# Optimization experiments

Measured on AMD Instinct MI355X. Metric: run time of the kernel, lower is better.

## Reference

```python
import jax, jax.numpy as jnp
import numpy as np

B, S, E, H, DH, W = 2, 4096, 1024, 16, 64, 512
NB = S // W          # number of query blocks
U = 2 * W            # key block = previous block + current block
INIT = 0.02


def setup_inputs() -> dict:
    key = jax.random.key(0)
    ks = jax.random.split(key, 6)
    x = jax.random.normal(ks[0], (B, S, E), jnp.float32)
    bias = jax.random.normal(ks[1], (H, W), jnp.float32)  # per-head alibi over rel. distance 0..W-1
    Wq = INIT * jax.random.normal(ks[2], (E, H, DH), jnp.float32)
    Wk = INIT * jax.random.normal(ks[3], (E, DH), jnp.float32)   # MQA: single shared K head
    Wv = INIT * jax.random.normal(ks[4], (E, DH), jnp.float32)   # MQA: single shared V head
    Wo = INIT * jax.random.normal(ks[5], (H, DH, E), jnp.float32)
    return {"x": x, "bias": bias, "Wq": Wq, "Wk": Wk, "Wv": Wv, "Wo": Wo}


def _sliding_window_attn(q, k, v, bias):
    # q: [B,S,H,DH]; k,v: [B,S,DH] (shared across heads); bias: [H,W]
    scale = 1.0 / np.sqrt(DH)
    qb = q.reshape(B, NB, W, H, DH)
    # pad one window of zeros in front so every query block sees a 'previous' block
    kp = jnp.pad(k, ((0, 0), (W, 0), (0, 0)))
    vp = jnp.pad(v, ((0, 0), (W, 0), (0, 0)))
    idx = jnp.arange(NB)[:, None] * W + jnp.arange(U)[None, :]  # [NB,U] into padded seq
    kb = kp[:, idx]  # [B,NB,U,DH]
    vb = vp[:, idx]  # [B,NB,U,DH]
    # scores over (query-in-block w, key-in-2W-block u)
    scores = jnp.einsum('bnwhd,bnud->bhnwu', qb, kb) * scale  # [B,H,NB,W,U]
    t = jnp.arange(W)
    u = jnp.arange(U)
    d = t[:, None] - u[None, :] + W                 # relative distance i-j, [W,U]
    rel_ok = (d >= 0) & (d < W)                     # causal + within window
    j_global = idx - W                              # global key position, [NB,U]
    valid = rel_ok[None, :, :] & (j_global >= 0)[:, None, :]  # [NB,W,U]
    bmat = bias[:, jnp.clip(d, 0, W - 1)]           # [H,W,U]
    scores = scores + bmat[None, :, None, :, :]
    neg = jnp.finfo(scores.dtype).min / 2
    scores = jnp.where(valid[None, None], scores, neg)
    p = jax.nn.softmax(scores, axis=-1)
    out = jnp.einsum('bhnwu,bnud->bnwhd', p, vb)    # [B,NB,W,H,DH]
    return out.reshape(B, S, H, DH)


def reference(x, bias, Wq, Wk, Wv, Wo):
    q = jnp.einsum('bse,ehd->bshd', x, Wq)
    k = jnp.einsum('bse,ed->bsd', x, Wk)
    v = jnp.einsum('bse,ed->bsd', x, Wv)
    attn = _sliding_window_attn(q, k, v, bias)
    return jnp.einsum('bshd,hde->bse', attn, Wo)
```

## Files before the change

kernel.cpp:

```cpp
#include <hip/hip_runtime.h>

#define Bx 2
#define Sx 4096
#define Ex 1024
#define Hx 16
#define DHx 64
#define Wwin 512

typedef unsigned short u16;
typedef unsigned int u32;
typedef __attribute__((ext_vector_type(8))) short bf16x8;
typedef __attribute__((ext_vector_type(4))) float f32x4;
typedef __attribute__((ext_vector_type(4))) unsigned short u16x4;

__device__ __forceinline__ u16 f2b(float f) {
  unsigned u = __builtin_bit_cast(unsigned, f);
  unsigned r = (u + 0x7FFFu + ((u >> 16) & 1u)) >> 16;
  return (u16)r;
}

__device__ __forceinline__ u32 cvt_pk_bf16(float lo, float hi) {
  u32 r;
  asm("v_cvt_pk_bf16_f32 %0, %1, %2" : "=v"(r) : "v"(lo), "v"(hi));
  return r;
}

__device__ __forceinline__ void gload_lds16(const void* g, void* l) {
  __builtin_amdgcn_global_load_lds(
      (const __attribute__((address_space(1))) void*)g,
      (__attribute__((address_space(3))) void*)l, 16, 0, 0);
}

__global__ __launch_bounds__(256) void cast_x_kernel(const float* __restrict__ x,
                                                     u16* __restrict__ xb) {
  long idx = ((long)blockIdx.x * 256 + threadIdx.x) * 4;
  float4 v = *(const float4*)(x + idx);
  u16x4 o;
  o[0] = f2b(v.x); o[1] = f2b(v.y); o[2] = f2b(v.z); o[3] = f2b(v.w);
  *(u16x4*)(xb + idx) = o;
}

__global__ __launch_bounds__(256) void pack_w_kernel(const float* __restrict__ Wq,
                                                     const float* __restrict__ Wk,
                                                     const float* __restrict__ Wv,
                                                     const float* __restrict__ Wo,
                                                     u16* __restrict__ wcat,
                                                     u16* __restrict__ wot) {
  int idx = blockIdx.x * 256 + threadIdx.x;
  if (idx < 1048576) {
    int e = idx >> 10, n = idx & 1023;
    wcat[n * 1024 + e] = f2b(Wq[idx]);
  } else if (idx < 1048576 + 65536) {
    int i2 = idx - 1048576;
    int e = i2 >> 6, d = i2 & 63;
    wcat[(1024 + d) * 1024 + e] = f2b(Wk[i2]);
  } else if (idx < 1048576 + 131072) {
    int i2 = idx - (1048576 + 65536);
    int e = i2 >> 6, d = i2 & 63;
    wcat[(1088 + d) * 1024 + e] = f2b(Wv[i2]);
  } else {
    int i2 = idx - (1048576 + 131072);
    int hd = i2 >> 10, e = i2 & 1023;
    wot[e * 1024 + hd] = f2b(Wo[i2]);
  }
}

template <typename OutT>
__global__ __launch_bounds__(256) void gemm_bt_kernel(const u16* __restrict__ A,
                                                      const u16* __restrict__ Bt,
                                                      OutT* __restrict__ C,
                                                      int M, int N, int K) {
  __shared__ u16 As[128 * 64];
  __shared__ u16 Bs[128 * 64];
  const int tid = threadIdx.x;
  const int lane = tid & 63, wave = tid >> 6;
  const int ll = lane & 15, gl = lane >> 4;
  const int wr = wave >> 1, wc = wave & 1;
  const long m0 = (long)blockIdx.x * 128;
  const long n0 = (long)blockIdx.y * 128;
  const int segrow = lane >> 3, cph = lane & 7;

  f32x4 acc[4][4] = {};

  for (int kb = 0; kb < K; kb += 64) {
    __syncthreads();
#pragma unroll
    for (int q = 0; q < 4; ++q) {
      int s = wave * 4 + q;
      int row = s * 8 + segrow;
      int clog = cph ^ (row & 7);
      gload_lds16(A + (m0 + row) * K + kb + clog * 8, (char*)As + s * 1024);
      gload_lds16(Bt + (n0 + row) * K + kb + clog * 8, (char*)Bs + s * 1024);
    }
    __syncthreads();
#pragma unroll
    for (int kx = 0; kx < 2; ++kx) {
      bf16x8 af[4], bfr[4];
#pragma unroll
      for (int rg = 0; rg < 4; ++rg) {
        int row = wr * 64 + rg * 16 + ll;
        int c = kx * 4 + gl;
        af[rg] = *(const bf16x8*)&As[row * 64 + ((c ^ (row & 7)) << 3)];
      }
#pragma unroll
      for (int cg = 0; cg < 4; ++cg) {
        int row = wc * 64 + cg * 16 + ll;
        int c = kx * 4 + gl;
        bfr[cg] = *(const bf16x8*)&Bs[row * 64 + ((c ^ (row & 7)) << 3)];
      }
#pragma unroll
      for (int rg = 0; rg < 4; ++rg)
#pragma unroll
        for (int cg = 0; cg < 4; ++cg)
          acc[rg][cg] = __builtin_amdgcn_mfma_f32_16x16x32_bf16(af[rg], bfr[cg],
                                                                acc[rg][cg], 0, 0, 0);
    }
  }
#pragma unroll
  for (int rg = 0; rg < 4; ++rg)
#pragma unroll
    for (int cg = 0; cg < 4; ++cg)
#pragma unroll
      for (int r = 0; r < 4; ++r) {
        long row = m0 + wr * 64 + rg * 16 + gl * 4 + r;
        long col = n0 + wc * 64 + cg * 16 + ll;
        if constexpr (sizeof(OutT) == 2)
          C[row * (long)N + col] = f2b(acc[rg][cg][r]);
        else
          C[row * (long)N + col] = acc[rg][cg][r];
      }
}

__global__ __launch_bounds__(256) void vt_transpose_kernel(const u16* __restrict__ qkvb,
                                                           u16* __restrict__ vt) {
  __shared__ u16 T[64 * 65];
  const int blk = blockIdx.x;
  const int b = blk >> 6;
  const int j0 = (blk & 63) * 64;
  const int tid = threadIdx.x;
#pragma unroll
  for (int rep = 0; rep < 16; ++rep) {
    int idx = rep * 256 + tid;
    int jj = idx >> 6, dd = idx & 63;
    T[dd * 65 + jj] = qkvb[((long)b * Sx + j0 + jj) * 1152 + 1088 + dd];
  }
  __syncthreads();
#pragma unroll
  for (int rep = 0; rep < 16; ++rep) {
    int idx = rep * 256 + tid;
    int dd = idx >> 6, jj = idx & 63;
    vt[((long)b * 64 + dd) * Sx + j0 + jj] = T[dd * 65 + jj];
  }
}

__global__ __launch_bounds__(256) void attn_kernel(const u16* __restrict__ qkv,
                                                   const u16* __restrict__ vt,
                                                   const float* __restrict__ bias,
                                                   u16* __restrict__ attnb) {
  __shared__ u16 Pb[4][32 * 64];
  __shared__ float bias2S[512];

  const int bid0 = blockIdx.x;
  const int bid = (bid0 & 7) * 128 + (bid0 >> 3);
  const int h = bid & 15;
  const int qt = (bid >> 4) & 31;
  const int b = bid >> 9;
  const int q0 = qt * 128;
  const long bS = (long)b * Sx;

  const int tid = threadIdx.x;
  const int lane = tid & 63, wave = tid >> 6;
  const int ll = lane & 15, gl = lane >> 4;
  const int wq0 = q0 + wave * 32;

  for (int i = tid; i < 512; i += 256)
    bias2S[i] = fmaf(bias[h * 512 + i], 1.4426950408889634f, -24.0f);
  __syncthreads();

  const float C1 = 0.125f * 1.4426950408889634f;

  bf16x8 qf[2][2];
#pragma unroll
  for (int rg = 0; rg < 2; ++rg)
#pragma unroll
    for (int kx = 0; kx < 2; ++kx)
      qf[rg][kx] = *(const bf16x8*)&qkv[(bS + wq0 + rg * 16 + ll) * 1152 +
                                        h * 64 + kx * 32 + gl * 8];

  u16 ov = (ll == 0) ? (u16)0x3F80 : (u16)0;
  bf16x8 vones;
#pragma unroll
  for (int i = 0; i < 8; ++i) vones[i] = (short)ov;

  f32x4 oacc[2][4] = {};
  f32x4 lacc[2] = {};

  u16* Pw = &Pb[wave][0];

  const int kb_start = (wq0 > 511) ? ((wq0 - 511) & ~63) : 0;
  const int kb_last = (wq0 + 31) & ~63;
  for (int kb = kb_start; kb <= kb_last; kb += 64) {
    bf16x8 kf[2][4], vfr[2][4];
#pragma unroll
    for (int kx = 0; kx < 2; ++kx)
#pragma unroll
      for (int cg = 0; cg < 4; ++cg) {
        kf[kx][cg] = *(const bf16x8*)&qkv[(bS + kb + cg * 16 + ll) * 1152 + 1024 +
                                          kx * 32 + gl * 8];
        vfr[kx][cg] = *(const bf16x8*)&vt[((long)b * 64 + cg * 16 + ll) * Sx + kb +
                                          kx * 32 + gl * 8];
      }
    f32x4 sacc[2][4] = {};
#pragma unroll
    for (int kx = 0; kx < 2; ++kx)
#pragma unroll
      for (int rg = 0; rg < 2; ++rg)
#pragma unroll
        for (int cg = 0; cg < 4; ++cg)
          sacc[rg][cg] = __builtin_amdgcn_mfma_f32_16x16x32_bf16(qf[rg][kx], kf[kx][cg],
                                                                 sacc[rg][cg], 0, 0, 0);
    const int dbase = (wq0 - kb) + gl * 4 - ll;
    const bool full = (kb - wq0 >= -480) && (kb - wq0 <= -64);
    if (full) {
      const float* bp = bias2S + dbase;
#pragma unroll
      for (int rg = 0; rg < 2; ++rg)
#pragma unroll
        for (int cg = 0; cg < 4; ++cg)
#pragma unroll
          for (int r = 0; r < 4; ++r)
            sacc[rg][cg][r] =
                __builtin_exp2f(fmaf(sacc[rg][cg][r], C1, bp[rg * 16 + r - cg * 16]));
    } else {
#pragma unroll
      for (int rg = 0; rg < 2; ++rg)
#pragma unroll
        for (int cg = 0; cg < 4; ++cg)
#pragma unroll
          for (int r = 0; r < 4; ++r) {
            int d = dbase + rg * 16 + r - cg * 16;
            int dc = d < 0 ? 0 : (d > 511 ? 511 : d);
            float p = __builtin_exp2f(fmaf(sacc[rg][cg][r], C1, bias2S[dc]));
            sacc[rg][cg][r] = ((unsigned)d < 512u) ? p : 0.0f;
          }
    }
#pragma unroll
    for (int rg = 0; rg < 2; ++rg)
#pragma unroll
      for (int cg = 0; cg < 4; ++cg)
#pragma unroll
        for (int rp = 0; rp < 2; ++rp) {
          u32 pk = cvt_pk_bf16(sacc[rg][cg][2 * rp], sacc[rg][cg][2 * rp + 1]);
          int row0 = rg * 16 + gl * 4 + 2 * rp;
          int col = cg * 16 + ll;
          Pw[row0 * 64 + (((col >> 3) ^ (row0 & 7)) << 3) + (col & 7)] = (u16)pk;
          int row1 = row0 + 1;
          Pw[row1 * 64 + (((col >> 3) ^ (row1 & 7)) << 3) + (col & 7)] = (u16)(pk >> 16);
        }
#pragma unroll
    for (int kx = 0; kx < 2; ++kx) {
      bf16x8 pf[2];
#pragma unroll
      for (int rg = 0; rg < 2; ++rg) {
        int row = rg * 16 + ll;
        int c = kx * 4 + gl;
        pf[rg] = *(const bf16x8*)&Pw[row * 64 + ((c ^ (row & 7)) << 3)];
      }
#pragma unroll
      for (int rg = 0; rg < 2; ++rg) {
#pragma unroll
        for (int cg = 0; cg < 4; ++cg)
          oacc[rg][cg] = __builtin_amdgcn_mfma_f32_16x16x32_bf16(pf[rg], vfr[kx][cg],
                                                                 oacc[rg][cg], 0, 0, 0);
        lacc[rg] = __builtin_amdgcn_mfma_f32_16x16x32_bf16(pf[rg], vones,
                                                           lacc[rg], 0, 0, 0);
      }
    }
  }
#pragma unroll
  for (int rg = 0; rg < 2; ++rg)
#pragma unroll
    for (int r = 0; r < 4; ++r) {
      float l = __shfl(lacc[rg][r], lane & 48);
      float inv = 1.0f / l;
      long i = wq0 + rg * 16 + gl * 4 + r;
#pragma unroll
      for (int cg = 0; cg < 4; ++cg)
        attnb[(bS + i) * 1024 + h * 64 + cg * 16 + ll] = f2b(oacc[rg][cg][r] * inv);
    }
}

extern "C" void kernel_launch(void* const* d_in, const int* in_sizes, int n_in,
                              void* d_out, int out_size, void* d_ws, size_t ws_size,
                              hipStream_t stream) {
  const float* x    = (const float*)d_in[0];
  const float* bias = (const float*)d_in[1];
  const float* Wq   = (const float*)d_in[2];
  const float* Wk   = (const float*)d_in[3];
  const float* Wv   = (const float*)d_in[4];
  const float* Wo   = (const float*)d_in[5];
  float* out = (float*)d_out;

  u16* xb    = (u16*)d_ws;
  u16* wcat  = xb    + (size_t)8192 * 1024;
  u16* wot   = wcat  + (size_t)1152 * 1024;
  u16* qkvb  = wot   + (size_t)1024 * 1024;
  u16* vtb   = qkvb  + (size_t)8192 * 1152;
  u16* attnb = xb;

  cast_x_kernel<<<8192, 256, 0, stream>>>(x, xb);
  pack_w_kernel<<<8704, 256, 0, stream>>>(Wq, Wk, Wv, Wo, wcat, wot);
  gemm_bt_kernel<u16><<<dim3(64, 9), 256, 0, stream>>>(xb, wcat, qkvb, 8192, 1152, 1024);
  vt_transpose_kernel<<<128, 256, 0, stream>>>(qkvb, vtb);
  attn_kernel<<<1024, 256, 0, stream>>>(qkvb, vtb, bias, attnb);
  gemm_bt_kernel<float><<<dim3(64, 8), 256, 0, stream>>>(attnb, wot, out, 8192, 1024, 1024);
}
```

Measured before the change: 231.0 us.

## Double-buffer GEMM LDS tiles and stage shared K/V tiles through LDS in attention

```diff
diff --git a/kernel.cpp b/kernel.cpp
--- a/kernel.cpp
+++ b/kernel.cpp
@@ -70,8 +70,8 @@
                                                       const u16* __restrict__ Bt,
                                                       OutT* __restrict__ C,
                                                       int M, int N, int K) {
-  __shared__ u16 As[128 * 64];
-  __shared__ u16 Bs[128 * 64];
+  __shared__ u16 As[2][128 * 64];
+  __shared__ u16 Bs[2][128 * 64];
   const int tid = threadIdx.x;
   const int lane = tid & 63, wave = tid >> 6;
   const int ll = lane & 15, gl = lane >> 4;
@@ -81,18 +81,26 @@
   const int segrow = lane >> 3, cph = lane & 7;
 
   f32x4 acc[4][4] = {};
-
-  for (int kb = 0; kb < K; kb += 64) {
-    __syncthreads();
-#pragma unroll
-    for (int q = 0; q < 4; ++q) {
-      int s = wave * 4 + q;
-      int row = s * 8 + segrow;
-      int clog = cph ^ (row & 7);
-      gload_lds16(A + (m0 + row) * K + kb + clog * 8, (char*)As + s * 1024);
-      gload_lds16(Bt + (n0 + row) * K + kb + clog * 8, (char*)Bs + s * 1024);
-    }
-    __syncthreads();
+  const int nt = K >> 6;
+
+#define GEMM_STAGE(buf, kb)                                                     \
+  {                                                                             \
+    _Pragma("unroll") for (int q = 0; q < 4; ++q) {                             \
+      int s = wave * 4 + q;                                                     \
+      int row = s * 8 + segrow;                                                 \
+      int clog = cph ^ (row & 7);                                               \
+      gload_lds16(A + (m0 + row) * K + (kb) + clog * 8,                         \
+                  (char*)&As[buf][0] + s * 1024);                               \
+      gload_lds16(Bt + (n0 + row) * K + (kb) + clog * 8,                        \
+                  (char*)&Bs[buf][0] + s * 1024);                               \
+    }                                                                           \
+  }
+
+  GEMM_STAGE(0, 0);
+  __syncthreads();
+  int cur = 0;
+  for (int t = 0; t < nt; ++t) {
+    if (t + 1 < nt) GEMM_STAGE(cur ^ 1, (t + 1) * 64);
 #pragma unroll
     for (int kx = 0; kx < 2; ++kx) {
       bf16x8 af[4], bfr[4];
@@ -100,13 +108,13 @@
       for (int rg = 0; rg < 4; ++rg) {
         int row = wr * 64 + rg * 16 + ll;
         int c = kx * 4 + gl;
-        af[rg] = *(const bf16x8*)&As[row * 64 + ((c ^ (row & 7)) << 3)];
+        af[rg] = *(const bf16x8*)&As[cur][row * 64 + ((c ^ (row & 7)) << 3)];
       }
 #pragma unroll
       for (int cg = 0; cg < 4; ++cg) {
         int row = wc * 64 + cg * 16 + ll;
         int c = kx * 4 + gl;
-        bfr[cg] = *(const bf16x8*)&Bs[row * 64 + ((c ^ (row & 7)) << 3)];
+        bfr[cg] = *(const bf16x8*)&Bs[cur][row * 64 + ((c ^ (row & 7)) << 3)];
       }
 #pragma unroll
       for (int rg = 0; rg < 4; ++rg)
@@ -115,7 +123,10 @@
           acc[rg][cg] = __builtin_amdgcn_mfma_f32_16x16x32_bf16(af[rg], bfr[cg],
                                                                 acc[rg][cg], 0, 0, 0);
     }
-  }
+    __syncthreads();
+    cur ^= 1;
+  }
+#undef GEMM_STAGE
 #pragma unroll
   for (int rg = 0; rg < 4; ++rg)
 #pragma unroll
@@ -157,6 +168,8 @@
                                                    const u16* __restrict__ vt,
                                                    const float* __restrict__ bias,
                                                    u16* __restrict__ attnb) {
+  __shared__ u16 Ks[2][64 * 64];
+  __shared__ u16 Vts[2][64 * 64];
   __shared__ u16 Pb[4][32 * 64];
   __shared__ float bias2S[512];
 
@@ -172,10 +185,10 @@
   const int lane = tid & 63, wave = tid >> 6;
   const int ll = lane & 15, gl = lane >> 4;
   const int wq0 = q0 + wave * 32;
+  const int segrow = lane >> 3, cph = lane & 7;
 
   for (int i = tid; i < 512; i += 256)
     bias2S[i] = fmaf(bias[h * 512 + i], 1.4426950408889634f, -24.0f);
-  __syncthreads();
 
   const float C1 = 0.125f * 1.4426950408889634f;
 
@@ -197,86 +210,114 @@
 
   u16* Pw = &Pb[wave][0];
 
-  const int kb_start = (wq0 > 511) ? ((wq0 - 511) & ~63) : 0;
-  const int kb_last = (wq0 + 31) & ~63;
-  for (int kb = kb_start; kb <= kb_last; kb += 64) {
-    bf16x8 kf[2][4], vfr[2][4];
-#pragma unroll
-    for (int kx = 0; kx < 2; ++kx)
-#pragma unroll
-      for (int cg = 0; cg < 4; ++cg) {
-        kf[kx][cg] = *(const bf16x8*)&qkv[(bS + kb + cg * 16 + ll) * 1152 + 1024 +
-                                          kx * 32 + gl * 8];
-        vfr[kx][cg] = *(const bf16x8*)&vt[((long)b * 64 + cg * 16 + ll) * Sx + kb +
-                                          kx * 32 + gl * 8];
-      }
-    f32x4 sacc[2][4] = {};
-#pragma unroll
-    for (int kx = 0; kx < 2; ++kx)
+#define ATTN_STAGE(buf, kb)                                                     \
+  {                                                                             \
+    _Pragma("unroll") for (int q = 0; q < 2; ++q) {                             \
+      int s = wave * 2 + q;                                                     \
+      int rrow = s * 8 + segrow;                    \
+      int clog = cph ^ (rrow & 7);                                              \
+      gload_lds16(qkv + (bS + (kb) + rrow) * 1152 + 1024 + clog * 8,            \
+                  (char*)&Ks[buf][0] + s * 1024);                               \
+      gload_lds16(vt + ((long)b * 64 + rrow) * Sx + (kb) + clog * 8,            \
+                  (char*)&Vts[buf][0] + s * 1024);                              \
+    }                                                                           \
+  }
+
+  const int kb_start = (q0 > 511) ? (q0 - 512) : 0;
+  const int kb_end = q0 + 64;
+  ATTN_STAGE(0, kb_start);
+  __syncthreads();
+  int cur = 0;
+  for (int kb = kb_start; kb <= kb_end; kb += 64) {
+    if (kb + 64 <= kb_end) ATTN_STAGE(cur ^ 1, kb + 64);
+    const bool active = (kb <= wq0 + 31) && (kb + 63 >= wq0 - 511);
+    if (active) {
+      f32x4 sacc[2][4] = {};
+#pragma unroll
+      for (int kx = 0; kx < 2; ++kx) {
+        bf16x8 kf[4];
+#pragma unroll
+        for (int cg = 0; cg < 4; ++cg) {
+          int key = cg * 16 + ll;
+          int c = kx * 4 + gl;
+          kf[cg] = *(const bf16x8*)&Ks[cur][key * 64 + ((c ^ (key & 7)) << 3)];
+        }
+#pragma unroll
+        for (int rg = 0; rg < 2; ++rg)
+#pragma unroll
+          for (int cg = 0; cg < 4; ++cg)
+            sacc[rg][cg] = __builtin_amdgcn_mfma_f32_16x16x32_bf16(qf[rg][kx], kf[cg],
+                                                                   sacc[rg][cg], 0, 0, 0);
+      }
+      const int dbase = (wq0 - kb) + gl * 4 - ll;
+      const bool full = (kb - wq0 >= -480) && (kb - wq0 <= -64);
+      if (full) {
+        const float* bp = bias2S + dbase;
+#pragma unroll
+        for (int rg = 0; rg < 2; ++rg)
+#pragma unroll
+          for (int cg = 0; cg < 4; ++cg)
+#pragma unroll
+            for (int r = 0; r < 4; ++r)
+              sacc[rg][cg][r] =
+                  __builtin_exp2f(fmaf(sacc[rg][cg][r], C1, bp[rg * 16 + r - cg * 16]));
+      } else {
+#pragma unroll
+        for (int rg = 0; rg < 2; ++rg)
+#pragma unroll
+          for (int cg = 0; cg < 4; ++cg)
+#pragma unroll
+            for (int r = 0; r < 4; ++r) {
+              int d = dbase + rg * 16 + r - cg * 16;
+              int dc = d < 0 ? 0 : (d > 511 ? 511 : d);
+              float p = __builtin_exp2f(fmaf(sacc[rg][cg][r], C1, bias2S[dc]));
+              sacc[rg][cg][r] = ((unsigned)d < 512u) ? p : 0.0f;
+            }
+      }
 #pragma unroll
       for (int rg = 0; rg < 2; ++rg)
 #pragma unroll
         for (int cg = 0; cg < 4; ++cg)
-          sacc[rg][cg] = __builtin_amdgcn_mfma_f32_16x16x32_bf16(qf[rg][kx], kf[kx][cg],
-                                                                 sacc[rg][cg], 0, 0, 0);
-    const int dbase = (wq0 - kb) + gl * 4 - ll;
-    const bool full = (kb - wq0 >= -480) && (kb - wq0 <= -64);
-    if (full) {
-      const float* bp = bias2S + dbase;
-#pragma unroll
-      for (int rg = 0; rg < 2; ++rg)
-#pragma unroll
-        for (int cg = 0; cg < 4; ++cg)
-#pragma unroll
-          for (int r = 0; r < 4; ++r)
-            sacc[rg][cg][r] =
-                __builtin_exp2f(fmaf(sacc[rg][cg][r], C1, bp[rg * 16 + r - cg * 16]));
-    } else {
-#pragma unroll
-      for (int rg = 0; rg < 2; ++rg)
-#pragma unroll
-        for (int cg = 0; cg < 4; ++cg)
-#pragma unroll
-          for (int r = 0; r < 4; ++r) {
-            int d = dbase + rg * 16 + r - cg * 16;
-            int dc = d < 0 ? 0 : (d > 511 ? 511 : d);
-            float p = __builtin_exp2f(fmaf(sacc[rg][cg][r], C1, bias2S[dc]));
-            sacc[rg][cg][r] = ((unsigned)d < 512u) ? p : 0.0f;
+#pragma unroll
+          for (int rp = 0; rp < 2; ++rp) {
+            u32 pk = cvt_pk_bf16(sacc[rg][cg][2 * rp], sacc[rg][cg][2 * rp + 1]);
+            int row0 = rg * 16 + gl * 4 + 2 * rp;
+            int col = cg * 16 + ll;
+            Pw[row0 * 64 + (((col >> 3) ^ (row0 & 7)) << 3) + (col & 7)] = (u16)pk;
+            int row1 = row0 + 1;
+            Pw[row1 * 64 + (((col >> 3) ^ (row1 & 7)) << 3) + (col & 7)] =
+                (u16)(pk >> 16);
           }
+#pragma unroll
+      for (int kx = 0; kx < 2; ++kx) {
+        bf16x8 pf[2], vf[4];
+#pragma unroll
+        for (int rg = 0; rg < 2; ++rg) {
+          int row = rg * 16 + ll;
+          int c = kx * 4 + gl;
+          pf[rg] = *(const bf16x8*)&Pw[row * 64 + ((c ^ (row & 7)) << 3)];
+        }
+#pragma unroll
+        for (int cg = 0; cg < 4; ++cg) {
+          int dh = cg * 16 + ll;
+          int c = kx * 4 + gl;
+          vf[cg] = *(const bf16x8*)&Vts[cur][dh * 64 + ((c ^ (dh & 7)) << 3)];
+        }
+#pragma unroll
+        for (int rg = 0; rg < 2; ++rg) {
+#pragma unroll
+          for (int cg = 0; cg < 4; ++cg)
+            oacc[rg][cg] = __builtin_amdgcn_mfma_f32_16x16x32_bf16(pf[rg], vf[cg],
+                                                                   oacc[rg][cg], 0, 0, 0);
+          lacc[rg] = __builtin_amdgcn_mfma_f32_16x16x32_bf16(pf[rg], vones,
+                                                             lacc[rg], 0, 0, 0);
+        }
+      }
     }
-#pragma unroll
-    for (int rg = 0; rg < 2; ++rg)
-#pragma unroll
-      for (int cg = 0; cg < 4; ++cg)
-#pragma unroll
-        for (int rp = 0; rp < 2; ++rp) {
-          u32 pk = cvt_pk_bf16(sacc[rg][cg][2 * rp], sacc[rg][cg][2 * rp + 1]);
-          int row0 = rg * 16 + gl * 4 + 2 * rp;
-          int col = cg * 16 + ll;
-          Pw[row0 * 64 + (((col >> 3) ^ (row0 & 7)) << 3) + (col & 7)] = (u16)pk;
-          int row1 = row0 + 1;
-          Pw[row1 * 64 + (((col >> 3) ^ (row1 & 7)) << 3) + (col & 7)] = (u16)(pk >> 16);
-        }
-#pragma unroll
-    for (int kx = 0; kx < 2; ++kx) {
-      bf16x8 pf[2];
-#pragma unroll
-      for (int rg = 0; rg < 2; ++rg) {
-        int row = rg * 16 + ll;
-        int c = kx * 4 + gl;
-        pf[rg] = *(const bf16x8*)&Pw[row * 64 + ((c ^ (row & 7)) << 3)];
-      }
-#pragma unroll
-      for (int rg = 0; rg < 2; ++rg) {
-#pragma unroll
-        for (int cg = 0; cg < 4; ++cg)
-          oacc[rg][cg] = __builtin_amdgcn_mfma_f32_16x16x32_bf16(pf[rg], vfr[kx][cg],
-                                                                 oacc[rg][cg], 0, 0, 0);
-        lacc[rg] = __builtin_amdgcn_mfma_f32_16x16x32_bf16(pf[rg], vones,
-                                                           lacc[rg], 0, 0, 0);
-      }
-    }
-  }
+    __syncthreads();
+    cur ^= 1;
+  }
+#undef ATTN_STAGE
 #pragma unroll
   for (int rg = 0; rg < 2; ++rg)
 #pragma unroll
```

Result: faster. 220.8 us (-4.4%).

## Stage shared K/V tiles in LDS with double buffering and use 32x32 MFMA

Applied to the files above, without the earlier changes.

```diff
diff --git a/kernel.cpp b/kernel.cpp
--- a/kernel.cpp
+++ b/kernel.cpp
@@ -11,6 +11,8 @@
 typedef unsigned int u32;
 typedef __attribute__((ext_vector_type(8))) short bf16x8;
 typedef __attribute__((ext_vector_type(4))) float f32x4;
+typedef __attribute__((ext_vector_type(16))) float f32x16;
+typedef __attribute__((ext_vector_type(4))) int i32x4;
 typedef __attribute__((ext_vector_type(4))) unsigned short u16x4;
 
 __device__ __forceinline__ u16 f2b(float f) {
@@ -157,7 +159,8 @@
                                                    const u16* __restrict__ vt,
                                                    const float* __restrict__ bias,
                                                    u16* __restrict__ attnb) {
-  __shared__ u16 Pb[4][32 * 64];
+  __shared__ u16 Ks[2][64 * 64];
+  __shared__ u16 Vts[2][64 * 64];
   __shared__ float bias2S[512];
 
   const int bid0 = blockIdx.x;
@@ -170,124 +173,122 @@
 
   const int tid = threadIdx.x;
   const int lane = tid & 63, wave = tid >> 6;
-  const int ll = lane & 15, gl = lane >> 4;
+  const int ql = lane & 31;
+  const int hi = lane >> 5;
   const int wq0 = q0 + wave * 32;
+  const int segrow = lane >> 3, cph = lane & 7;
 
   for (int i = tid; i < 512; i += 256)
     bias2S[i] = fmaf(bias[h * 512 + i], 1.4426950408889634f, -24.0f);
+
+  const float C1 = 0.125f * 1.4426950408889634f;
+
+  bf16x8 qf[4];
+#pragma unroll
+  for (int s = 0; s < 4; ++s)
+    qf[s] = *(const bf16x8*)&qkv[(bS + wq0 + ql) * 1152 + h * 64 + s * 16 + hi * 8];
+
+  bf16x8 vones;
+#pragma unroll
+  for (int i = 0; i < 8; ++i) vones[i] = (short)0x3F80;
+
+  f32x16 oacc[2] = {};
+  f32x16 lacc = {};
+
+#define ATTN_STAGE(buf, kb)                                                     \
+  {                                                                             \
+    _Pragma("unroll") for (int q = 0; q < 2; ++q) {                             \
+      int s = wave * 2 + q;                                                     \
+      int rrow = s * 8 + segrow;                    \
+      int clog = cph ^ (rrow & 7);                                              \
+      gload_lds16(qkv + (bS + (kb) + rrow) * 1152 + 1024 + clog * 8,            \
+                  (char*)&Ks[buf][0] + s * 1024);                               \
+      gload_lds16(vt + ((long)b * 64 + rrow) * Sx + (kb) + clog * 8,            \
+                  (char*)&Vts[buf][0] + s * 1024);                              \
+    }                                                                           \
+  }
+
+  const int kb_start = (q0 > 511) ? (q0 - 512) : 0;
+  const int kb_end = q0 + 64;
+  ATTN_STAGE(0, kb_start);
   __syncthreads();
-
-  const float C1 = 0.125f * 1.4426950408889634f;
-
-  bf16x8 qf[2][2];
-#pragma unroll
-  for (int rg = 0; rg < 2; ++rg)
-#pragma unroll
-    for (int kx = 0; kx < 2; ++kx)
-      qf[rg][kx] = *(const bf16x8*)&qkv[(bS + wq0 + rg * 16 + ll) * 1152 +
-                                        h * 64 + kx * 32 + gl * 8];
-
-  u16 ov = (ll == 0) ? (u16)0x3F80 : (u16)0;
-  bf16x8 vones;
-#pragma unroll
-  for (int i = 0; i < 8; ++i) vones[i] = (short)ov;
-
-  f32x4 oacc[2][4] = {};
-  f32x4 lacc[2] = {};
-
-  u16* Pw = &Pb[wave][0];
-
-  const int kb_start = (wq0 > 511) ? ((wq0 - 511) & ~63) : 0;
-  const int kb_last = (wq0 + 31) & ~63;
-  for (int kb = kb_start; kb <= kb_last; kb += 64) {
-    bf16x8 kf[2][4], vfr[2][4];
-#pragma unroll
-    for (int kx = 0; kx < 2; ++kx)
-#pragma unroll
-      for (int cg = 0; cg < 4; ++cg) {
-        kf[kx][cg] = *(const bf16x8*)&qkv[(bS + kb + cg * 16 + ll) * 1152 + 1024 +
-                                          kx * 32 + gl * 8];
-        vfr[kx][cg] = *(const bf16x8*)&vt[((long)b * 64 + cg * 16 + ll) * Sx + kb +
-                                          kx * 32 + gl * 8];
-      }
-    f32x4 sacc[2][4] = {};
-#pragma unroll
-    for (int kx = 0; kx < 2; ++kx)
-#pragma unroll
-      for (int rg = 0; rg < 2; ++rg)
-#pragma unroll
-        for (int cg = 0; cg < 4; ++cg)
-          sacc[rg][cg] = __builtin_amdgcn_mfma_f32_16x16x32_bf16(qf[rg][kx], kf[kx][cg],
-                                                                 sacc[rg][cg], 0, 0, 0);
-    const int dbase = (wq0 - kb) + gl * 4 - ll;
-    const bool full = (kb - wq0 >= -480) && (kb - wq0 <= -64);
-    if (full) {
-      const float* bp = bias2S + dbase;
-#pragma unroll
-      for (int rg = 0; rg < 2; ++rg)
-#pragma unroll
-        for (int cg = 0; cg < 4; ++cg)
-#pragma unroll
-          for (int r = 0; r < 4; ++r)
-            sacc[rg][cg][r] =
-                __builtin_exp2f(fmaf(sacc[rg][cg][r], C1, bp[rg * 16 + r - cg * 16]));
-    } else {
-#pragma unroll
-      for (int rg = 0; rg < 2; ++rg)
-#pragma unroll
-        for (int cg = 0; cg < 4; ++cg)
-#pragma unroll
-          for (int r = 0; r < 4; ++r) {
-            int d = dbase + rg * 16 + r - cg * 16;
+  int cur = 0;
+  for (int kb = kb_start; kb <= kb_end; kb += 64) {
+    if (kb + 64 <= kb_end) ATTN_STAGE(cur ^ 1, kb + 64);
+    const bool active = (kb <= wq0 + 31) && (kb + 63 >= wq0 - 511);
+    if (active) {
+      f32x16 sacc[2] = {};
+#pragma unroll
+      for (int kblk = 0; kblk < 2; ++kblk) {
+        int key = kblk * 32 + ql;
+#pragma unroll
+        for (int s = 0; s < 4; ++s) {
+          int c = 2 * s + hi;
+          bf16x8 kf = *(const bf16x8*)&Ks[cur][key * 64 + ((c ^ (key & 7)) << 3)];
+          sacc[kblk] = __builtin_amdgcn_mfma_f32_32x32x16_bf16(kf, qf[s],
+                                                               sacc[kblk], 0, 0, 0);
+        }
+      }
+      const int dbase = wq0 + ql - kb - 4 * hi;
+      const bool full = (kb - wq0 >= -480) && (kb - wq0 <= -64);
+      if (full) {
+        const float* bpz = bias2S + dbase - 63;
+#pragma unroll
+        for (int kblk = 0; kblk < 2; ++kblk)
+#pragma unroll
+          for (int r = 0; r < 16; ++r) {
+            const int off = kblk * 32 + (r & 3) + 8 * (r >> 2);
+            sacc[kblk][r] = __builtin_exp2f(fmaf(sacc[kblk][r], C1, bpz[63 - off]));
+          }
+      } else {
+#pragma unroll
+        for (int kblk = 0; kblk < 2; ++kblk)
+#pragma unroll
+          for (int r = 0; r < 16; ++r) {
+            const int off = kblk * 32 + (r & 3) + 8 * (r >> 2);
+            int d = dbase - off;
             int dc = d < 0 ? 0 : (d > 511 ? 511 : d);
-            float p = __builtin_exp2f(fmaf(sacc[rg][cg][r], C1, bias2S[dc]));
-            sacc[rg][cg][r] = ((unsigned)d < 512u) ? p : 0.0f;
+            float p = __builtin_exp2f(fmaf(sacc[kblk][r], C1, bias2S[dc]));
+            sacc[kblk][r] = ((unsigned)d < 512u) ? p : 0.0f;
           }
+      }
+#pragma unroll
+      for (int s = 0; s < 4; ++s) {
+        const int kblk = s >> 1;
+        const int m0 = 2 * (s & 1);
+        u32 a0 = cvt_pk_bf16(sacc[kblk][4 * m0 + 0], sacc[kblk][4 * m0 + 1]);
+        u32 a1 = cvt_pk_bf16(sacc[kblk][4 * m0 + 2], sacc[kblk][4 * m0 + 3]);
+        u32 b0 = cvt_pk_bf16(sacc[kblk][4 * m0 + 4], sacc[kblk][4 * m0 + 5]);
+        u32 b1 = cvt_pk_bf16(sacc[kblk][4 * m0 + 6], sacc[kblk][4 * m0 + 7]);
+        asm("v_permlane32_swap_b32 %0, %1" : "+v"(a0), "+v"(b0));
+        asm("v_permlane32_swap_b32 %0, %1" : "+v"(a1), "+v"(b1));
+        i32x4 t;
+        t.x = (int)a0; t.y = (int)a1; t.z = (int)b0; t.w = (int)b1;
+        bf16x8 pa = __builtin_bit_cast(bf16x8, t);
+        lacc = __builtin_amdgcn_mfma_f32_32x32x16_bf16(pa, vones, lacc, 0, 0, 0);
+#pragma unroll
+        for (int dhblk = 0; dhblk < 2; ++dhblk) {
+          int dh = dhblk * 32 + ql;
+          int c = 2 * s + hi;
+          bf16x8 vf = *(const bf16x8*)&Vts[cur][dh * 64 + ((c ^ (dh & 7)) << 3)];
+          oacc[dhblk] = __builtin_amdgcn_mfma_f32_32x32x16_bf16(pa, vf,
+                                                                oacc[dhblk], 0, 0, 0);
+        }
+      }
     }
-#pragma unroll
-    for (int rg = 0; rg < 2; ++rg)
-#pragma unroll
-      for (int cg = 0; cg < 4; ++cg)
-#pragma unroll
-        for (int rp = 0; rp < 2; ++rp) {
-          u32 pk = cvt_pk_bf16(sacc[rg][cg][2 * rp], sacc[rg][cg][2 * rp + 1]);
-          int row0 = rg * 16 + gl * 4 + 2 * rp;
-          int col = cg * 16 + ll;
-          Pw[row0 * 64 + (((col >> 3) ^ (row0 & 7)) << 3) + (col & 7)] = (u16)pk;
-          int row1 = row0 + 1;
-          Pw[row1 * 64 + (((col >> 3) ^ (row1 & 7)) << 3) + (col & 7)] = (u16)(pk >> 16);
-        }
-#pragma unroll
-    for (int kx = 0; kx < 2; ++kx) {
-      bf16x8 pf[2];
-#pragma unroll
-      for (int rg = 0; rg < 2; ++rg) {
-        int row = rg * 16 + ll;
-        int c = kx * 4 + gl;
-        pf[rg] = *(const bf16x8*)&Pw[row * 64 + ((c ^ (row & 7)) << 3)];
-      }
-#pragma unroll
-      for (int rg = 0; rg < 2; ++rg) {
-#pragma unroll
-        for (int cg = 0; cg < 4; ++cg)
-          oacc[rg][cg] = __builtin_amdgcn_mfma_f32_16x16x32_bf16(pf[rg], vfr[kx][cg],
-                                                                 oacc[rg][cg], 0, 0, 0);
-        lacc[rg] = __builtin_amdgcn_mfma_f32_16x16x32_bf16(pf[rg], vones,
-                                                           lacc[rg], 0, 0, 0);
-      }
-    }
-  }
-#pragma unroll
-  for (int rg = 0; rg < 2; ++rg)
-#pragma unroll
-    for (int r = 0; r < 4; ++r) {
-      float l = __shfl(lacc[rg][r], lane & 48);
-      float inv = 1.0f / l;
-      long i = wq0 + rg * 16 + gl * 4 + r;
-#pragma unroll
-      for (int cg = 0; cg < 4; ++cg)
-        attnb[(bS + i) * 1024 + h * 64 + cg * 16 + ll] = f2b(oacc[rg][cg][r] * inv);
-    }
+    __syncthreads();
+    cur ^= 1;
+  }
+#undef ATTN_STAGE
+#pragma unroll
+  for (int r = 0; r < 16; ++r) {
+    const int q = (r & 3) + 8 * (r >> 2) + 4 * hi;
+    float inv = 1.0f / lacc[r];
+    long row = (bS + wq0 + q) * 1024 + h * 64;
+#pragma unroll
+    for (int dhblk = 0; dhblk < 2; ++dhblk)
+      attnb[row + dhblk * 32 + ql] = f2b(oacc[dhblk][r] * inv);
+  }
 }
 
 extern "C" void kernel_launch(void* const* d_in, const int* in_sizes, int n_in,
```

New measurement: 208.9 us. -9.6%, faster.
